# Kernel optimization log

Measured on AMD Instinct MI355X. Metric: run time of the kernel, lower is better.

The kernel has to match this reference:

```python
import jax, jax.numpy as jnp
import numpy as np

B, T = 128, 64          # batch, episode length
OB, AC, L, H = 32, 8, 128, 256  # ob_dim, ac_dim, latent_dim, mlp hidden
N_SUB = 4               # fixed Dopri5 substeps per interval (replaces adaptive PID controller)


def setup_inputs() -> dict:
    key = jax.random.key(0)
    ks = jax.random.split(key, 12)
    g = lambda k, shape, fan: jax.random.normal(k, shape, jnp.float32) / np.sqrt(fan)
    return {
        "ob": jax.random.normal(ks[0], (B, OB), jnp.float32),
        "acs": jax.random.normal(ks[1], (B, T, AC), jnp.float32),
        # strictly increasing timestamps (cumsum of uniform increments)
        "times": jnp.cumsum(jax.random.uniform(ks[2], (B, T), jnp.float32, 0.02, 0.1), axis=1),
        # ob encoder MLP (OB -> H -> L), relu hidden, identity out
        "We0": g(ks[3], (H, OB), OB), "be0": jnp.zeros((H,), jnp.float32),
        "We1": g(ks[4], (L, H), H), "be1": jnp.zeros((L,), jnp.float32),
        # latent dynamics MLP (L -> H -> H -> L)
        "Wd0": g(ks[5], (H, L), L), "bd0": jnp.zeros((H,), jnp.float32),
        "Wd1": g(ks[6], (H, H), H), "bd1": jnp.zeros((H,), jnp.float32),
        "Wd2": g(ks[7], (L, H), H), "bd2": jnp.zeros((L,), jnp.float32),
        # ob decoder MLP (L -> H -> OB)
        "Wo0": g(ks[8], (H, L), L), "bo0": jnp.zeros((H,), jnp.float32),
        "Wo1": g(ks[9], (OB, H), H), "bo1": jnp.zeros((OB,), jnp.float32),
        # GRU cell (input=AC, hidden=L), equinox layout: gates [r, z, n]
        "Wih": g(ks[10], (3 * L, AC), AC), "Whh": g(ks[11], (3 * L, L), L),
        "bih": jnp.zeros((3 * L,), jnp.float32), "bn": jnp.zeros((L,), jnp.float32),
    }


def reference(ob, acs, times, We0, be0, We1, be1, Wd0, bd0, Wd1, bd1, Wd2, bd2,
              Wo0, bo0, Wo1, bo1, Wih, Whh, bih, bn):
    def f(y):  # dynamics MLP on batched latent (B, L) -> (B, L)
        h1 = jax.nn.relu(y @ Wd0.T + bd0)
        h2 = jax.nn.relu(h1 @ Wd1.T + bd1)
        return h2 @ Wd2.T + bd2

    def gru(x, h):  # equinox GRUCell math, batched
        ir, iz, inn = jnp.split(x @ Wih.T + bih, 3, axis=-1)
        hr, hz, hn = jnp.split(h @ Whh.T, 3, axis=-1)
        r = jax.nn.sigmoid(ir + hr)
        z = jax.nn.sigmoid(iz + hz)
        n = jnp.tanh(inn + r * (hn + bn))
        return (1.0 - z) * n + z * h

    def dopri5_step(y, h):  # one Dopri5 (RK45) step, h: (B, 1) per-sample step size
        k1 = f(y)
        k2 = f(y + h * (0.2 * k1))
        k3 = f(y + h * (3/40 * k1 + 9/40 * k2))
        k4 = f(y + h * (44/45 * k1 - 56/15 * k2 + 32/9 * k3))
        k5 = f(y + h * (19372/6561 * k1 - 25360/2187 * k2 + 64448/6561 * k3 - 212/729 * k4))
        k6 = f(y + h * (9017/3168 * k1 - 355/33 * k2 + 46732/5247 * k3 + 49/176 * k4 - 5103/18656 * k5))
        return y + h * (35/384 * k1 + 500/1113 * k3 + 125/192 * k4 - 2187/6784 * k5 + 11/84 * k6)

    def integrate(y, dt):  # integrate latent ODE from 0 to dt with N_SUB fixed Dopri5 steps
        h = (dt / N_SUB)[:, None]
        return jax.lax.fori_loop(0, N_SUB, lambda i, yy: dopri5_step(yy, h), y)

    # encode first observation, consume first action
    latent0 = jax.nn.relu(ob @ We0.T + be0) @ We1.T + be1  # (B, L)
    latent0 = gru(acs[:, 0], latent0)

    dts = jnp.diff(times, axis=1)  # (B, T-1)

    def step(latent, xs):
        ac, dt = xs
        latent = integrate(latent, dt)
        latent = gru(ac, latent)
        return latent, latent

    xs = (jnp.swapaxes(acs[:, 1:], 0, 1), dts.T)  # time-major for scan
    _, lat_seq = jax.lax.scan(step, latent0, xs)  # (T-1, B, L)

    latents = jnp.concatenate([latent0[None], lat_seq], axis=0)  # (T, B, L)
    latents = jnp.swapaxes(latents, 0, 1)  # (B, T, L)

    h1 = jax.nn.relu(latents @ Wo0.T + bo0)
    return h1 @ Wo1.T + bo1  # (B, T, OB)
```

## Files before the change

kernel.cpp:

```cpp
#include <hip/hip_runtime.h>
#include <stdint.h>

#define NBATCH 128
#define NT     64
#define OBD    32
#define ACD    8
#define LDIM   128
#define HDIM   256

typedef _Float16 h2 __attribute__((ext_vector_type(2)));
typedef float    f4 __attribute__((ext_vector_type(4)));

#if defined(__has_builtin)
#  if __has_builtin(__builtin_amdgcn_fdot2)
#    define HAVE_FDOT2 1
#  endif
#endif

__device__ __forceinline__ float dot2f(h2 a, h2 b, float c) {
#ifdef HAVE_FDOT2
  return __builtin_amdgcn_fdot2(a, b, c, false);
#else
  return c + (float)a[0] * (float)b[0] + (float)a[1] * (float)b[1];
#endif
}

__device__ __forceinline__ h2 pkh(float a, float b) {
  h2 r; r[0] = (_Float16)a; r[1] = (_Float16)b; return r;
}

__device__ __forceinline__ h2 bch(float x) { return __builtin_bit_cast(h2, x); }
__device__ __forceinline__ float fch(h2 x) { return __builtin_bit_cast(float, x); }

__device__ __forceinline__ float sigmf(float x) { return 1.0f / (1.0f + expf(-x)); }

__global__ void prep_w1(const float* __restrict__ Wd1, f4* __restrict__ ws4) {
  int idx = blockIdx.x * blockDim.x + threadIdx.x;
  int j  = idx >> 9;
  int tt = idx & 511;
  const float* src = Wd1 + (2 * (tt >> 2) + (j & 1)) * HDIM
                         + (tt & 3) * 64 + (j >> 1) * 8;
  f4 c;
  c.x = fch(pkh(src[0], src[1]));
  c.y = fch(pkh(src[2], src[3]));
  c.z = fch(pkh(src[4], src[5]));
  c.w = fch(pkh(src[6], src[7]));
  ws4[j * 512 + tt] = c;
}

__global__ __attribute__((amdgpu_waves_per_eu(2, 2))) __launch_bounds__(512)
void ode_rnn_kernel(const float* __restrict__ ob,   const float* __restrict__ acs,
                    const float* __restrict__ times,
                    const float* __restrict__ We0,  const float* __restrict__ be0,
                    const float* __restrict__ We1,  const float* __restrict__ be1,
                    const float* __restrict__ Wd0,  const float* __restrict__ bd0,
                    const float* __restrict__ bd1,
                    const float* __restrict__ Wd2,  const float* __restrict__ bd2,
                    const float* __restrict__ Wo0,  const float* __restrict__ bo0,
                    const float* __restrict__ Wo1,  const float* __restrict__ bo1,
                    const float* __restrict__ Wih,  const float* __restrict__ Whh,
                    const float* __restrict__ bih,  const float* __restrict__ bn,
                    const f4* __restrict__ ws4,
                    float* __restrict__ out)
{
  const int t  = threadIdx.x;
  const int b  = blockIdx.x;
  const int G1 = t >> 2, K1 = t & 3;
  const int G3 = t >> 3, K3 = t & 7;
  const int p   = t >> 1;
  const int sub = t & 1;

  __shared__ __align__(16) float s_lat[LDIM];
  __shared__ __align__(16) float s_gz[LDIM];
  __shared__ __align__(16) float s_gin[LDIM];
  __shared__ __align__(16) float s_ghn[LDIM];
  __shared__ __align__(16) float s_tmp[HDIM];
  __shared__ __align__(16) float s_obs[OBD];
  __shared__ __align__(16) float s_times[NT];
  __shared__ __align__(16) float s_acs[NT * ACD];
  __shared__ __align__(16) h2    s_in16[96];
  __shared__ __align__(16) h2    s_a16[152];
  __shared__ __align__(16) h2    s_b16[160];

  h2 w0[32], w2[32];
  {
    const float2* r0 = (const float2*)(Wd0 + (2 * G1) * LDIM + K1 * 32);
    const float2* r1 = (const float2*)(Wd0 + (2 * G1 + 1) * LDIM + K1 * 32);
#pragma unroll
    for (int i = 0; i < 16; ++i) {
      float2 u = r0[i], v = r1[i];
      w0[i] = pkh(u.x, u.y); w0[16 + i] = pkh(v.x, v.y);
    }
  }
  {
    const float2* r0 = (const float2*)(Wd2 + (2 * G3) * HDIM + K3 * 32);
    const float2* r1 = (const float2*)(Wd2 + (2 * G3 + 1) * HDIM + K3 * 32);
#pragma unroll
    for (int i = 0; i < 16; ++i) {
      float2 u = r0[i], v = r1[i];
      w2[i] = pkh(u.x, u.y); w2[16 + i] = pkh(v.x, v.y);
    }
  }
  const f4* wsb = ws4 + t;

  const float bb00 = bd0[2 * G1], bb01 = bd0[2 * G1 + 1];
  const float bb10 = bd1[2 * G1], bb11 = bd1[2 * G1 + 1];
  const float bb20 = bd2[2 * G3], bb21 = bd2[2 * G3 + 1];
  const float rb0  = bo0[p];
  const float gA   = (t < 3 * LDIM) ? bih[t] : 0.0f;
  const float bnr  = (t < LDIM) ? bn[t] : 0.0f;

  float latr0 = 0.0f, latr1 = 0.0f;

  auto substep = [&](float hs) {
    float k00 = 0, k10 = 0, k20 = 0, k30 = 0, k40 = 0;
    float k01 = 0, k11 = 0, k21 = 0, k31 = 0, k41 = 0;
#pragma unroll
    for (int s = 0; s < 6; ++s) {
      f4 y0 = wsb[0 * 512], y1 = wsb[1 * 512];
      f4 y2 = wsb[2 * 512], y3 = wsb[3 * 512];
      float a0, a1, b0, b1, v0, v1;
      a0 = a1 = b0 = b1 = 0.0f;
      {
        const f4* act = ((const f4*)s_in16) + K1 * 6;
#pragma unroll
        for (int i = 0; i < 4; ++i) {
          f4 q = act[i];
          a0 = dot2f(w0[4*i+0], bch(q.x), a0);
          a1 = dot2f(w0[4*i+1], bch(q.y), a1);
          a0 = dot2f(w0[4*i+2], bch(q.z), a0);
          a1 = dot2f(w0[4*i+3], bch(q.w), a1);
          b0 = dot2f(w0[16+4*i+0], bch(q.x), b0);
          b1 = dot2f(w0[16+4*i+1], bch(q.y), b1);
          b0 = dot2f(w0[16+4*i+2], bch(q.z), b0);
          b1 = dot2f(w0[16+4*i+3], bch(q.w), b1);
        }
      }
      v0 = a0 + a1; v1 = b0 + b1;
      v0 += __shfl_xor(v0, 1); v0 += __shfl_xor(v0, 2);
      v1 += __shfl_xor(v1, 1); v1 += __shfl_xor(v1, 2);
      v0 = fmaxf(v0 + bb00, 0.0f); v1 = fmaxf(v1 + bb01, 0.0f);
      if (K1 == 0) s_a16[(G1 >> 5) * 40 + (G1 & 31)] = pkh(v0, v1);
      __syncthreads();
      a0 = a1 = b0 = b1 = 0.0f;
      {
        const f4* act = ((const f4*)s_a16) + K1 * 10;
        f4 q;
#define SD2(W0V, W1V, J) q = act[J]; \
        a0 = dot2f(bch(W0V.x), bch(q.x), a0); \
        a1 = dot2f(bch(W0V.y), bch(q.y), a1); \
        a0 = dot2f(bch(W0V.z), bch(q.z), a0); \
        a1 = dot2f(bch(W0V.w), bch(q.w), a1); \
        b0 = dot2f(bch(W1V.x), bch(q.x), b0); \
        b1 = dot2f(bch(W1V.y), bch(q.y), b1); \
        b0 = dot2f(bch(W1V.z), bch(q.z), b0); \
        b1 = dot2f(bch(W1V.w), bch(q.w), b1);
        f4 y4 = wsb[4 * 512],  y5 = wsb[5 * 512];
        SD2(y0, y1, 0)
        f4 y6 = wsb[6 * 512],  y7 = wsb[7 * 512];
        SD2(y2, y3, 1)
        f4 y8 = wsb[8 * 512],  y9 = wsb[9 * 512];
        SD2(y4, y5, 2)
        f4 y10 = wsb[10 * 512], y11 = wsb[11 * 512];
        SD2(y6, y7, 3)
        f4 y12 = wsb[12 * 512], y13 = wsb[13 * 512];
        SD2(y8, y9, 4)
        f4 y14 = wsb[14 * 512], y15 = wsb[15 * 512];
        SD2(y10, y11, 5)
        SD2(y12, y13, 6)
        SD2(y14, y15, 7)
#undef SD2
      }
      v0 = a0 + a1; v1 = b0 + b1;
      v0 += __shfl_xor(v0, 1); v0 += __shfl_xor(v0, 2);
      v1 += __shfl_xor(v1, 1); v1 += __shfl_xor(v1, 2);
      v0 = fmaxf(v0 + bb10, 0.0f); v1 = fmaxf(v1 + bb11, 0.0f);
      if (K1 == 0) s_b16[(G1 >> 4) * 20 + (G1 & 15)] = pkh(v0, v1);
      __syncthreads();
      a0 = a1 = b0 = b1 = 0.0f;
      {
        const f4* act = ((const f4*)s_b16) + K3 * 5;
#pragma unroll
        for (int i = 0; i < 4; ++i) {
          f4 q = act[i];
          a0 = dot2f(w2[4*i+0], bch(q.x), a0);
          a1 = dot2f(w2[4*i+1], bch(q.y), a1);
          a0 = dot2f(w2[4*i+2], bch(q.z), a0);
          a1 = dot2f(w2[4*i+3], bch(q.w), a1);
          b0 = dot2f(w2[16+4*i+0], bch(q.x), b0);
          b1 = dot2f(w2[16+4*i+1], bch(q.y), b1);
          b0 = dot2f(w2[16+4*i+2], bch(q.z), b0);
          b1 = dot2f(w2[16+4*i+3], bch(q.w), b1);
        }
      }
      v0 = a0 + a1; v1 = b0 + b1;
      v0 += __shfl_xor(v0, 1); v0 += __shfl_xor(v0, 2); v0 += __shfl_xor(v0, 4);
      v1 += __shfl_xor(v1, 1); v1 += __shfl_xor(v1, 2); v1 += __shfl_xor(v1, 4);
      float kv0 = v0 + bb20, kv1 = v1 + bb21;
      float z0, z1;
      if (s == 0) {
        k00 = kv0; k01 = kv1;
        z0 = latr0 + hs * (0.2f * kv0);
        z1 = latr1 + hs * (0.2f * kv1);
      } else if (s == 1) {
        k10 = kv0; k11 = kv1;
        z0 = latr0 + hs * ((3.0f/40.0f)*k00 + (9.0f/40.0f)*kv0);
        z1 = latr1 + hs * ((3.0f/40.0f)*k01 + (9.0f/40.0f)*kv1);
      } else if (s == 2) {
        k20 = kv0; k21 = kv1;
        z0 = latr0 + hs * ((44.0f/45.0f)*k00 - (56.0f/15.0f)*k10 + (32.0f/9.0f)*kv0);
        z1 = latr1 + hs * ((44.0f/45.0f)*k01 - (56.0f/15.0f)*k11 + (32.0f/9.0f)*kv1);
      } else if (s == 3) {
        k30 = kv0; k31 = kv1;
        z0 = latr0 + hs * ((19372.0f/6561.0f)*k00 - (25360.0f/2187.0f)*k10
                         + (64448.0f/6561.0f)*k20 - (212.0f/729.0f)*kv0);
        z1 = latr1 + hs * ((19372.0f/6561.0f)*k01 - (25360.0f/2187.0f)*k11
                         + (64448.0f/6561.0f)*k21 - (212.0f/729.0f)*kv1);
      } else if (s == 4) {
        k40 = kv0; k41 = kv1;
        z0 = latr0 + hs * ((9017.0f/3168.0f)*k00 - (355.0f/33.0f)*k10
                         + (46732.0f/5247.0f)*k20 + (49.0f/176.0f)*k30
                         - (5103.0f/18656.0f)*kv0);
        z1 = latr1 + hs * ((9017.0f/3168.0f)*k01 - (355.0f/33.0f)*k11
                         + (46732.0f/5247.0f)*k21 + (49.0f/176.0f)*k31
                         - (5103.0f/18656.0f)*kv1);
      } else {
        z0 = latr0 + hs * ((35.0f/384.0f)*k00 + (500.0f/1113.0f)*k20
                         + (125.0f/192.0f)*k30 - (2187.0f/6784.0f)*k40
                         + (11.0f/84.0f)*kv0);
        z1 = latr1 + hs * ((35.0f/384.0f)*k01 + (500.0f/1113.0f)*k21
                         + (125.0f/192.0f)*k31 - (2187.0f/6784.0f)*k41
                         + (11.0f/84.0f)*kv1);
        latr0 = z0; latr1 = z1;
      }
      if (K3 == 0) {
        s_in16[(G3 >> 4) * 24 + (G3 & 15)] = pkh(z0, z1);
        if (s == 5) { s_lat[2*G3] = z0; s_lat[2*G3 + 1] = z1; }
      }
      __syncthreads();
    }
  };

  auto gru = [&](int ts) {
    __syncthreads();
    float vi = gA, vh = 0.0f;
    if (t < 3 * LDIM) {
      const float* xa = s_acs + ts * ACD;
      const f4* wiv = (const f4*)(Wih + t * ACD);
      f4 wa = wiv[0], wb = wiv[1];
      vi += wa.x*xa[0] + wa.y*xa[1] + wa.z*xa[2] + wa.w*xa[3]
          + wb.x*xa[4] + wb.y*xa[5] + wb.z*xa[6] + wb.w*xa[7];
      const f4* wh = (const f4*)(Whh + t * LDIM);
      const f4* xl = (const f4*)s_lat;
#pragma unroll
      for (int k2 = 0; k2 < LDIM / 4; ++k2) {
        f4 w = wh[k2], x = xl[k2];
        vh += w.x*x.x + w.y*x.y + w.z*x.z + w.w*x.w;
      }
    }
    if (t >= LDIM && t < 2 * LDIM)          s_gz[t - LDIM] = vi + vh;
    else if (t >= 2 * LDIM && t < 3 * LDIM) { s_gin[t - 2*LDIM] = vi; s_ghn[t - 2*LDIM] = vh; }
    __syncthreads();
    if (t < LDIM) {
      float rg = sigmf(vi + vh);
      float zg = sigmf(s_gz[t]);
      float ng = tanhf(s_gin[t] + rg * (s_ghn[t] + bnr));
      float y  = (1.0f - zg) * ng + zg * s_lat[t];
      s_lat[t] = y;
      float ov = __shfl_xor(y, 1);
      if (!(t & 1)) {
        int g = t >> 1;
        s_in16[(g >> 4) * 24 + (g & 15)] = pkh(y, ov);
      }
    }
  };

  auto decode = [&](int ts) {
    __syncthreads();
    { float2 ld = *(const float2*)(s_lat + 2 * G3); latr0 = ld.x; latr1 = ld.y; }
    float acc = 0.0f;
    {
      const f4* wr = (const f4*)(Wo0 + p * LDIM + sub * 64);
      const f4* xl = ((const f4*)s_lat) + sub * 16;
#pragma unroll
      for (int k2 = 0; k2 < 16; ++k2) {
        f4 w = wr[k2], x = xl[k2];
        acc += w.x*x.x + w.y*x.y + w.z*x.z + w.w*x.w;
      }
    }
    acc += __shfl_xor(acc, 1);
    acc = fmaxf(acc + rb0, 0.0f);
    { float ov = __shfl_xor(acc, 2);
      if ((t & 3) == 0) { int i = t >> 2; s_a16[i + ((i >> 6) << 2)] = pkh(acc, ov); } }
    __syncthreads();
    const int o  = t >> 4;
    const int sl = t & 15;
    float v2 = 0.0f;
    {
      const f4* wr = (const f4*)(Wo1 + o * HDIM + sl * 16);
      const h2* xs = s_a16 + sl * 8 + ((sl >> 3) << 2);
#pragma unroll
      for (int i = 0; i < 4; ++i) {
        f4 w = wr[i];
        h2 xa = xs[2*i], xb = xs[2*i+1];
        v2 += w.x*(float)xa[0] + w.y*(float)xa[1]
            + w.z*(float)xb[0] + w.w*(float)xb[1];
      }
    }
    v2 += __shfl_xor(v2, 1);
    v2 += __shfl_xor(v2, 2);
    v2 += __shfl_xor(v2, 4);
    v2 += __shfl_xor(v2, 8);
    if (sl == 0) out[((size_t)b * NT + ts) * OBD + o] = v2 + bo1[o];
    __syncthreads();
  };

  if (t < OBD) s_obs[t] = ob[b * OBD + t];
  if (t < NT)  s_times[t] = times[b * NT + t];
  s_acs[t] = acs[(size_t)b * NT * ACD + t];
  __syncthreads();
  if (t < HDIM) {
    float acc = be0[t];
    const float* wr = We0 + t * OBD;
#pragma unroll
    for (int j = 0; j < OBD; ++j) acc += wr[j] * s_obs[j];
    s_tmp[t] = fmaxf(acc, 0.0f);
  }
  __syncthreads();
  {
    const int rr = t >> 2, kk = t & 3;
    const f4* wr = (const f4*)(We1 + rr * HDIM + kk * 64);
    const f4* xs = ((const f4*)s_tmp) + kk * 16;
    float acc = 0.0f;
#pragma unroll
    for (int k = 0; k < 16; ++k) {
      f4 w = wr[k], x = xs[k];
      acc += w.x*x.x + w.y*x.y + w.z*x.z + w.w*x.w;
    }
    acc += __shfl_xor(acc, 1);
    acc += __shfl_xor(acc, 2);
    if (kk == 0) s_lat[rr] = acc + be1[rr];
  }

  gru(0);
  decode(0);

#pragma unroll 1
  for (int ts = 1; ts < NT; ++ts) {
    float hs = 0.25f * (s_times[ts] - s_times[ts - 1]);
#pragma unroll 1
    for (int su = 0; su < 4; ++su) substep(hs);
    gru(ts);
    decode(ts);
  }
}

extern "C" void kernel_launch(void* const* d_in, const int* in_sizes, int n_in,
                              void* d_out, int out_size, void* d_ws, size_t ws_size,
                              hipStream_t stream) {
  (void)in_sizes; (void)n_in; (void)ws_size; (void)out_size;
  const float* ob    = (const float*)d_in[0];
  const float* acs   = (const float*)d_in[1];
  const float* times = (const float*)d_in[2];
  const float* We0   = (const float*)d_in[3];
  const float* be0   = (const float*)d_in[4];
  const float* We1   = (const float*)d_in[5];
  const float* be1   = (const float*)d_in[6];
  const float* Wd0   = (const float*)d_in[7];
  const float* bd0   = (const float*)d_in[8];
  const float* Wd1   = (const float*)d_in[9];
  const float* bd1   = (const float*)d_in[10];
  const float* Wd2   = (const float*)d_in[11];
  const float* bd2   = (const float*)d_in[12];
  const float* Wo0   = (const float*)d_in[13];
  const float* bo0   = (const float*)d_in[14];
  const float* Wo1   = (const float*)d_in[15];
  const float* bo1   = (const float*)d_in[16];
  const float* Wih   = (const float*)d_in[17];
  const float* Whh   = (const float*)d_in[18];
  const float* bih   = (const float*)d_in[19];
  const float* bn    = (const float*)d_in[20];

  f4* ws4 = (f4*)d_ws;

  prep_w1<<<dim3(16), dim3(512), 0, stream>>>(Wd1, ws4);
  ode_rnn_kernel<<<dim3(NBATCH), dim3(512), 0, stream>>>(
      ob, acs, times, We0, be0, We1, be1, Wd0, bd0, bd1, Wd2, bd2,
      Wo0, bo0, Wo1, bo1, Wih, Whh, bih, bn, ws4, (float*)d_out);
}
```

Baseline: 2.368 ms.

## Double threads per batch block to 1024 and split each dot product further

Grows the per-batch block from 512 to 1024 threads. Each dynamics-MLP, GRU and encoder dot product is split across twice as many lanes, using extra shuffle reductions, and the prepacked Wd1 layout and shared-memory strides are rebuilt to match. The goal is shorter per-thread serial dependency chains in the latency-bound sequential ODE loop. The cost is more shuffles and more waves taking part in every __syncthreads barrier, while the decode stage leaves half the threads idle.

After: 3.109 ms. 1.31x slower.

```diff
diff --git a/kernel.cpp b/kernel.cpp
--- a/kernel.cpp
+++ b/kernel.cpp
@@ -36,19 +36,19 @@
 
 __global__ void prep_w1(const float* __restrict__ Wd1, f4* __restrict__ ws4) {
   int idx = blockIdx.x * blockDim.x + threadIdx.x;
-  int j  = idx >> 9;
-  int tt = idx & 511;
-  const float* src = Wd1 + (2 * (tt >> 2) + (j & 1)) * HDIM
-                         + (tt & 3) * 64 + (j >> 1) * 8;
+  int j  = idx >> 10;
+  int tt = idx & 1023;
+  const float* src = Wd1 + (2 * (tt >> 3) + (j & 1)) * HDIM
+                         + (tt & 7) * 32 + (j >> 1) * 8;
   f4 c;
   c.x = fch(pkh(src[0], src[1]));
   c.y = fch(pkh(src[2], src[3]));
   c.z = fch(pkh(src[4], src[5]));
   c.w = fch(pkh(src[6], src[7]));
-  ws4[j * 512 + tt] = c;
-}
-
-__global__ __attribute__((amdgpu_waves_per_eu(2, 2))) __launch_bounds__(512)
+  ws4[j * 1024 + tt] = c;
+}
+
+__global__ __attribute__((amdgpu_waves_per_eu(4, 4))) __launch_bounds__(1024)
 void ode_rnn_kernel(const float* __restrict__ ob,   const float* __restrict__ acs,
                     const float* __restrict__ times,
                     const float* __restrict__ We0,  const float* __restrict__ be0,
@@ -65,12 +65,11 @@
 {
   const int t  = threadIdx.x;
   const int b  = blockIdx.x;
-  const int G1 = t >> 2, K1 = t & 3;
-  const int G3 = t >> 3, K3 = t & 7;
-  const int p   = t >> 1;
-  const int sub = t & 1;
+  const int G1 = t >> 3, K1 = t & 7;
+  const int G3 = t >> 4, K3 = t & 15;
 
   __shared__ __align__(16) float s_lat[LDIM];
+  __shared__ __align__(16) float s_gr[LDIM];
   __shared__ __align__(16) float s_gz[LDIM];
   __shared__ __align__(16) float s_gin[LDIM];
   __shared__ __align__(16) float s_ghn[LDIM];
@@ -79,26 +78,26 @@
   __shared__ __align__(16) float s_times[NT];
   __shared__ __align__(16) float s_acs[NT * ACD];
   __shared__ __align__(16) h2    s_in16[96];
-  __shared__ __align__(16) h2    s_a16[152];
-  __shared__ __align__(16) h2    s_b16[160];
-
-  h2 w0[32], w2[32];
+  __shared__ __align__(16) h2    s_a16[160];
+  __shared__ __align__(16) h2    s_b16[192];
+
+  h2 w0[16], w2[16];
   {
-    const float2* r0 = (const float2*)(Wd0 + (2 * G1) * LDIM + K1 * 32);
-    const float2* r1 = (const float2*)(Wd0 + (2 * G1 + 1) * LDIM + K1 * 32);
-#pragma unroll
-    for (int i = 0; i < 16; ++i) {
+    const float2* r0 = (const float2*)(Wd0 + (2 * G1) * LDIM + K1 * 16);
+    const float2* r1 = (const float2*)(Wd0 + (2 * G1 + 1) * LDIM + K1 * 16);
+#pragma unroll
+    for (int i = 0; i < 8; ++i) {
       float2 u = r0[i], v = r1[i];
-      w0[i] = pkh(u.x, u.y); w0[16 + i] = pkh(v.x, v.y);
+      w0[i] = pkh(u.x, u.y); w0[8 + i] = pkh(v.x, v.y);
     }
   }
   {
-    const float2* r0 = (const float2*)(Wd2 + (2 * G3) * HDIM + K3 * 32);
-    const float2* r1 = (const float2*)(Wd2 + (2 * G3 + 1) * HDIM + K3 * 32);
-#pragma unroll
-    for (int i = 0; i < 16; ++i) {
+    const float2* r0 = (const float2*)(Wd2 + (2 * G3) * HDIM + K3 * 16);
+    const float2* r1 = (const float2*)(Wd2 + (2 * G3 + 1) * HDIM + K3 * 16);
+#pragma unroll
+    for (int i = 0; i < 8; ++i) {
       float2 u = r0[i], v = r1[i];
-      w2[i] = pkh(u.x, u.y); w2[16 + i] = pkh(v.x, v.y);
+      w2[i] = pkh(u.x, u.y); w2[8 + i] = pkh(v.x, v.y);
     }
   }
   const f4* wsb = ws4 + t;
@@ -106,8 +105,8 @@
   const float bb00 = bd0[2 * G1], bb01 = bd0[2 * G1 + 1];
   const float bb10 = bd1[2 * G1], bb11 = bd1[2 * G1 + 1];
   const float bb20 = bd2[2 * G3], bb21 = bd2[2 * G3 + 1];
-  const float rb0  = bo0[p];
-  const float gA   = (t < 3 * LDIM) ? bih[t] : 0.0f;
+  const float rb0  = (t < 512) ? bo0[t >> 1] : 0.0f;
+  const float gA   = (t < 768) ? bih[t >> 1] : 0.0f;
   const float bnr  = (t < LDIM) ? bn[t] : 0.0f;
 
   float latr0 = 0.0f, latr1 = 0.0f;
@@ -117,85 +116,75 @@
     float k01 = 0, k11 = 0, k21 = 0, k31 = 0, k41 = 0;
 #pragma unroll
     for (int s = 0; s < 6; ++s) {
-      f4 y0 = wsb[0 * 512], y1 = wsb[1 * 512];
-      f4 y2 = wsb[2 * 512], y3 = wsb[3 * 512];
+      f4 y0 = wsb[0 * 1024], y1 = wsb[1 * 1024];
+      f4 y2 = wsb[2 * 1024], y3 = wsb[3 * 1024];
       float a0, a1, b0, b1, v0, v1;
       a0 = a1 = b0 = b1 = 0.0f;
       {
-        const f4* act = ((const f4*)s_in16) + K1 * 6;
-#pragma unroll
-        for (int i = 0; i < 4; ++i) {
+        const f4* act = ((const f4*)s_in16) + K1 * 3;
+#pragma unroll
+        for (int i = 0; i < 2; ++i) {
           f4 q = act[i];
           a0 = dot2f(w0[4*i+0], bch(q.x), a0);
           a1 = dot2f(w0[4*i+1], bch(q.y), a1);
           a0 = dot2f(w0[4*i+2], bch(q.z), a0);
           a1 = dot2f(w0[4*i+3], bch(q.w), a1);
-          b0 = dot2f(w0[16+4*i+0], bch(q.x), b0);
-          b1 = dot2f(w0[16+4*i+1], bch(q.y), b1);
-          b0 = dot2f(w0[16+4*i+2], bch(q.z), b0);
-          b1 = dot2f(w0[16+4*i+3], bch(q.w), b1);
+          b0 = dot2f(w0[8+4*i+0], bch(q.x), b0);
+          b1 = dot2f(w0[8+4*i+1], bch(q.y), b1);
+          b0 = dot2f(w0[8+4*i+2], bch(q.z), b0);
+          b1 = dot2f(w0[8+4*i+3], bch(q.w), b1);
         }
       }
       v0 = a0 + a1; v1 = b0 + b1;
-      v0 += __shfl_xor(v0, 1); v0 += __shfl_xor(v0, 2);
-      v1 += __shfl_xor(v1, 1); v1 += __shfl_xor(v1, 2);
+      v0 += __shfl_xor(v0, 1); v0 += __shfl_xor(v0, 2); v0 += __shfl_xor(v0, 4);
+      v1 += __shfl_xor(v1, 1); v1 += __shfl_xor(v1, 2); v1 += __shfl_xor(v1, 4);
       v0 = fmaxf(v0 + bb00, 0.0f); v1 = fmaxf(v1 + bb01, 0.0f);
-      if (K1 == 0) s_a16[(G1 >> 5) * 40 + (G1 & 31)] = pkh(v0, v1);
+      if (K1 == 0) s_a16[(G1 >> 4) * 20 + (G1 & 15)] = pkh(v0, v1);
       __syncthreads();
       a0 = a1 = b0 = b1 = 0.0f;
       {
-        const f4* act = ((const f4*)s_a16) + K1 * 10;
+        const f4* act = ((const f4*)s_a16) + K1 * 5;
         f4 q;
-#define SD2(W0V, W1V, J) q = act[J]; \
-        a0 = dot2f(bch(W0V.x), bch(q.x), a0); \
-        a1 = dot2f(bch(W0V.y), bch(q.y), a1); \
-        a0 = dot2f(bch(W0V.z), bch(q.z), a0); \
-        a1 = dot2f(bch(W0V.w), bch(q.w), a1); \
-        b0 = dot2f(bch(W1V.x), bch(q.x), b0); \
-        b1 = dot2f(bch(W1V.y), bch(q.y), b1); \
-        b0 = dot2f(bch(W1V.z), bch(q.z), b0); \
-        b1 = dot2f(bch(W1V.w), bch(q.w), b1);
-        f4 y4 = wsb[4 * 512],  y5 = wsb[5 * 512];
-        SD2(y0, y1, 0)
-        f4 y6 = wsb[6 * 512],  y7 = wsb[7 * 512];
-        SD2(y2, y3, 1)
-        f4 y8 = wsb[8 * 512],  y9 = wsb[9 * 512];
-        SD2(y4, y5, 2)
-        f4 y10 = wsb[10 * 512], y11 = wsb[11 * 512];
-        SD2(y6, y7, 3)
-        f4 y12 = wsb[12 * 512], y13 = wsb[13 * 512];
-        SD2(y8, y9, 4)
-        f4 y14 = wsb[14 * 512], y15 = wsb[15 * 512];
-        SD2(y10, y11, 5)
-        SD2(y12, y13, 6)
-        SD2(y14, y15, 7)
-#undef SD2
+#define SD1(ACC0, ACC1, WV) \
+        ACC0 = dot2f(bch(WV.x), bch(q.x), ACC0); \
+        ACC1 = dot2f(bch(WV.y), bch(q.y), ACC1); \
+        ACC0 = dot2f(bch(WV.z), bch(q.z), ACC0); \
+        ACC1 = dot2f(bch(WV.w), bch(q.w), ACC1);
+        f4 y4 = wsb[4 * 1024], y5 = wsb[5 * 1024];
+        q = act[0]; SD1(a0, a1, y0) SD1(b0, b1, y1)
+        f4 y6 = wsb[6 * 1024], y7 = wsb[7 * 1024];
+        q = act[1]; SD1(a0, a1, y2) SD1(b0, b1, y3)
+        q = act[2]; SD1(a0, a1, y4) SD1(b0, b1, y5)
+        q = act[3]; SD1(a0, a1, y6) SD1(b0, b1, y7)
+#undef SD1
       }
       v0 = a0 + a1; v1 = b0 + b1;
-      v0 += __shfl_xor(v0, 1); v0 += __shfl_xor(v0, 2);
-      v1 += __shfl_xor(v1, 1); v1 += __shfl_xor(v1, 2);
+      v0 += __shfl_xor(v0, 1); v0 += __shfl_xor(v0, 2); v0 += __shfl_xor(v0, 4);
+      v1 += __shfl_xor(v1, 1); v1 += __shfl_xor(v1, 2); v1 += __shfl_xor(v1, 4);
       v0 = fmaxf(v0 + bb10, 0.0f); v1 = fmaxf(v1 + bb11, 0.0f);
-      if (K1 == 0) s_b16[(G1 >> 4) * 20 + (G1 & 15)] = pkh(v0, v1);
+      if (K1 == 0) s_b16[(G1 >> 3) * 12 + (G1 & 7)] = pkh(v0, v1);
       __syncthreads();
       a0 = a1 = b0 = b1 = 0.0f;
       {
-        const f4* act = ((const f4*)s_b16) + K3 * 5;
-#pragma unroll
-        for (int i = 0; i < 4; ++i) {
+        const f4* act = ((const f4*)s_b16) + K3 * 3;
+#pragma unroll
+        for (int i = 0; i < 2; ++i) {
           f4 q = act[i];
           a0 = dot2f(w2[4*i+0], bch(q.x), a0);
           a1 = dot2f(w2[4*i+1], bch(q.y), a1);
           a0 = dot2f(w2[4*i+2], bch(q.z), a0);
           a1 = dot2f(w2[4*i+3], bch(q.w), a1);
-          b0 = dot2f(w2[16+4*i+0], bch(q.x), b0);
-          b1 = dot2f(w2[16+4*i+1], bch(q.y), b1);
-          b0 = dot2f(w2[16+4*i+2], bch(q.z), b0);
-          b1 = dot2f(w2[16+4*i+3], bch(q.w), b1);
+          b0 = dot2f(w2[8+4*i+0], bch(q.x), b0);
+          b1 = dot2f(w2[8+4*i+1], bch(q.y), b1);
+          b0 = dot2f(w2[8+4*i+2], bch(q.z), b0);
+          b1 = dot2f(w2[8+4*i+3], bch(q.w), b1);
         }
       }
       v0 = a0 + a1; v1 = b0 + b1;
-      v0 += __shfl_xor(v0, 1); v0 += __shfl_xor(v0, 2); v0 += __shfl_xor(v0, 4);
-      v1 += __shfl_xor(v1, 1); v1 += __shfl_xor(v1, 2); v1 += __shfl_xor(v1, 4);
+      v0 += __shfl_xor(v0, 1); v0 += __shfl_xor(v0, 2);
+      v0 += __shfl_xor(v0, 4); v0 += __shfl_xor(v0, 8);
+      v1 += __shfl_xor(v1, 1); v1 += __shfl_xor(v1, 2);
+      v1 += __shfl_xor(v1, 4); v1 += __shfl_xor(v1, 8);
       float kv0 = v0 + bb20, kv1 = v1 + bb21;
       float z0, z1;
       if (s == 0) {
@@ -234,7 +223,7 @@
         latr0 = z0; latr1 = z1;
       }
       if (K3 == 0) {
-        s_in16[(G3 >> 4) * 24 + (G3 & 15)] = pkh(z0, z1);
+        s_in16[(G3 >> 3) * 12 + (G3 & 7)] = pkh(z0, z1);
         if (s == 5) { s_lat[2*G3] = z0; s_lat[2*G3 + 1] = z1; }
       }
       __syncthreads();
@@ -244,25 +233,30 @@
   auto gru = [&](int ts) {
     __syncthreads();
     float vi = gA, vh = 0.0f;
-    if (t < 3 * LDIM) {
-      const float* xa = s_acs + ts * ACD;
-      const f4* wiv = (const f4*)(Wih + t * ACD);
-      f4 wa = wiv[0], wb = wiv[1];
-      vi += wa.x*xa[0] + wa.y*xa[1] + wa.z*xa[2] + wa.w*xa[3]
-          + wb.x*xa[4] + wb.y*xa[5] + wb.z*xa[6] + wb.w*xa[7];
-      const f4* wh = (const f4*)(Whh + t * LDIM);
-      const f4* xl = (const f4*)s_lat;
-#pragma unroll
-      for (int k2 = 0; k2 < LDIM / 4; ++k2) {
+    const int gr = t >> 1, kh = t & 1;
+    if (t < 768) {
+      const float* xa = s_acs + ts * ACD + kh * 4;
+      const f4* wiv = (const f4*)(Wih + gr * ACD + kh * 4);
+      f4 wa = wiv[0];
+      vi += wa.x*xa[0] + wa.y*xa[1] + wa.z*xa[2] + wa.w*xa[3];
+      const f4* wh = (const f4*)(Whh + gr * LDIM + kh * 64);
+      const f4* xl = ((const f4*)s_lat) + kh * 16;
+#pragma unroll
+      for (int k2 = 0; k2 < 16; ++k2) {
         f4 w = wh[k2], x = xl[k2];
         vh += w.x*x.x + w.y*x.y + w.z*x.z + w.w*x.w;
       }
     }
-    if (t >= LDIM && t < 2 * LDIM)          s_gz[t - LDIM] = vi + vh;
-    else if (t >= 2 * LDIM && t < 3 * LDIM) { s_gin[t - 2*LDIM] = vi; s_ghn[t - 2*LDIM] = vh; }
+    vi += __shfl_xor(vi, 1);
+    vh += __shfl_xor(vh, 1);
+    if (t < 768 && kh == 0) {
+      if (gr < LDIM)           s_gr[gr] = vi + vh;
+      else if (gr < 2 * LDIM)  s_gz[gr - LDIM] = vi + vh;
+      else                   { s_gin[gr - 2*LDIM] = vi; s_ghn[gr - 2*LDIM] = vh; }
+    }
     __syncthreads();
     if (t < LDIM) {
-      float rg = sigmf(vi + vh);
+      float rg = sigmf(s_gr[t]);
       float zg = sigmf(s_gz[t]);
       float ng = tanhf(s_gin[t] + rg * (s_ghn[t] + bnr));
       float y  = (1.0f - zg) * ng + zg * s_lat[t];
@@ -270,7 +264,7 @@
       float ov = __shfl_xor(y, 1);
       if (!(t & 1)) {
         int g = t >> 1;
-        s_in16[(g >> 4) * 24 + (g & 15)] = pkh(y, ov);
+        s_in16[(g >> 3) * 12 + (g & 7)] = pkh(y, ov);
       }
     }
   };
@@ -278,46 +272,51 @@
   auto decode = [&](int ts) {
     __syncthreads();
     { float2 ld = *(const float2*)(s_lat + 2 * G3); latr0 = ld.x; latr1 = ld.y; }
-    float acc = 0.0f;
-    {
-      const f4* wr = (const f4*)(Wo0 + p * LDIM + sub * 64);
-      const f4* xl = ((const f4*)s_lat) + sub * 16;
-#pragma unroll
-      for (int k2 = 0; k2 < 16; ++k2) {
-        f4 w = wr[k2], x = xl[k2];
-        acc += w.x*x.x + w.y*x.y + w.z*x.z + w.w*x.w;
-      }
-    }
-    acc += __shfl_xor(acc, 1);
-    acc = fmaxf(acc + rb0, 0.0f);
-    { float ov = __shfl_xor(acc, 2);
-      if ((t & 3) == 0) { int i = t >> 2; s_a16[i + ((i >> 6) << 2)] = pkh(acc, ov); } }
-    __syncthreads();
-    const int o  = t >> 4;
-    const int sl = t & 15;
-    float v2 = 0.0f;
-    {
-      const f4* wr = (const f4*)(Wo1 + o * HDIM + sl * 16);
-      const h2* xs = s_a16 + sl * 8 + ((sl >> 3) << 2);
-#pragma unroll
-      for (int i = 0; i < 4; ++i) {
-        f4 w = wr[i];
-        h2 xa = xs[2*i], xb = xs[2*i+1];
-        v2 += w.x*(float)xa[0] + w.y*(float)xa[1]
-            + w.z*(float)xb[0] + w.w*(float)xb[1];
-      }
-    }
-    v2 += __shfl_xor(v2, 1);
-    v2 += __shfl_xor(v2, 2);
-    v2 += __shfl_xor(v2, 4);
-    v2 += __shfl_xor(v2, 8);
-    if (sl == 0) out[((size_t)b * NT + ts) * OBD + o] = v2 + bo1[o];
+    if (t < 512) {
+      const int p = t >> 1, sub = t & 1;
+      float acc = 0.0f;
+      {
+        const f4* wr = (const f4*)(Wo0 + p * LDIM + sub * 64);
+        const f4* xl = ((const f4*)s_lat) + sub * 16;
+#pragma unroll
+        for (int k2 = 0; k2 < 16; ++k2) {
+          f4 w = wr[k2], x = xl[k2];
+          acc += w.x*x.x + w.y*x.y + w.z*x.z + w.w*x.w;
+        }
+      }
+      acc += __shfl_xor(acc, 1);
+      acc = fmaxf(acc + rb0, 0.0f);
+      { float ov = __shfl_xor(acc, 2);
+        if ((t & 3) == 0) { int i = t >> 2; s_a16[i + ((i >> 6) << 2)] = pkh(acc, ov); } }
+    }
+    __syncthreads();
+    if (t < 512) {
+      const int o  = t >> 4;
+      const int sl = t & 15;
+      float v2 = 0.0f;
+      {
+        const f4* wr = (const f4*)(Wo1 + o * HDIM + sl * 16);
+        const h2* xs = s_a16 + sl * 8 + ((sl >> 3) << 2);
+#pragma unroll
+        for (int i = 0; i < 4; ++i) {
+          f4 w = wr[i];
+          h2 xa = xs[2*i], xb = xs[2*i+1];
+          v2 += w.x*(float)xa[0] + w.y*(float)xa[1]
+              + w.z*(float)xb[0] + w.w*(float)xb[1];
+        }
+      }
+      v2 += __shfl_xor(v2, 1);
+      v2 += __shfl_xor(v2, 2);
+      v2 += __shfl_xor(v2, 4);
+      v2 += __shfl_xor(v2, 8);
+      if (sl == 0) out[((size_t)b * NT + ts) * OBD + o] = v2 + bo1[o];
+    }
     __syncthreads();
   };
 
   if (t < OBD) s_obs[t] = ob[b * OBD + t];
   if (t < NT)  s_times[t] = times[b * NT + t];
-  s_acs[t] = acs[(size_t)b * NT * ACD + t];
+  if (t < NT * ACD) s_acs[t] = acs[(size_t)b * NT * ACD + t];
   __syncthreads();
   if (t < HDIM) {
     float acc = be0[t];
@@ -328,17 +327,18 @@
   }
   __syncthreads();
   {
-    const int rr = t >> 2, kk = t & 3;
-    const f4* wr = (const f4*)(We1 + rr * HDIM + kk * 64);
-    const f4* xs = ((const f4*)s_tmp) + kk * 16;
+    const int rr = t >> 3, kk = t & 7;
+    const f4* wr = (const f4*)(We1 + rr * HDIM + kk * 32);
+    const f4* xs = ((const f4*)s_tmp) + kk * 8;
     float acc = 0.0f;
 #pragma unroll
-    for (int k = 0; k < 16; ++k) {
+    for (int k = 0; k < 8; ++k) {
       f4 w = wr[k], x = xs[k];
       acc += w.x*x.x + w.y*x.y + w.z*x.z + w.w*x.w;
     }
     acc += __shfl_xor(acc, 1);
     acc += __shfl_xor(acc, 2);
+    acc += __shfl_xor(acc, 4);
     if (kk == 0) s_lat[rr] = acc + be1[rr];
   }
 
@@ -383,8 +383,8 @@
 
   f4* ws4 = (f4*)d_ws;
 
-  prep_w1<<<dim3(16), dim3(512), 0, stream>>>(Wd1, ws4);
-  ode_rnn_kernel<<<dim3(NBATCH), dim3(512), 0, stream>>>(
+  prep_w1<<<dim3(8), dim3(1024), 0, stream>>>(Wd1, ws4);
+  ode_rnn_kernel<<<dim3(NBATCH), dim3(1024), 0, stream>>>(
       ob, acs, times, We0, be0, We1, be1, Wd0, bd0, bd1, Wd2, bd2,
       Wo0, bo0, Wo1, bo1, Wih, Whh, bih, bn, ws4, (float*)d_out);
 }
```
